# Kernel optimization log

Hardware: AMD Instinct MI355X
Metric: run time of the kernel (lower is better)

## Reference

```python
import jax, jax.numpy as jnp
import numpy as np

LEVEL_N = [81920, 20480, 5120, 1280, 320]  # faces at div..div-4 (div=6, 20*4^d)
K = 10  # SpherePHD conv kernel taps
W_SHAPES = [(64,3),(64,64),(128,64),(128,128),(256,128),(256,256),(256,256),(512,256),(512,512),(512,512),(512,512),(512,512),(512,512)]
BLOCKS = [[0,1],[2,3],[4,5,6],[7,8,9],[10,11,12]]  # conv indices per VGG block


def setup_inputs() -> dict:
    key = jax.random.key(0)
    ks = iter(jax.random.split(key, 64))
    d = {"x": jax.random.normal(next(ks), (2, 3, LEVEL_N[0]), jnp.float32)}
    for l, n in enumerate(LEVEL_N):
        d[f"conv_t{l}"] = jax.random.randint(next(ks), (n, K), 0, n, jnp.int32)
        d[f"adj_t{l}"] = jax.random.randint(next(ks), (n, 4), 0, n, jnp.int32)
        d[f"pool_t{l}"] = jax.random.randint(next(ks), (n // 4,), 0, n, jnp.int32)
    for i, (o, c) in enumerate(W_SHAPES):
        d[f"w{i}"] = jax.random.normal(next(ks), (o, c, K), jnp.float32) * (1.0 / np.sqrt(c * K))
        d[f"b{i}"] = jnp.zeros((o,), jnp.float32)
    return d


def phd_conv(x, w, b, table):
    # x: [B,C,N], table: [N,K] -> gather neighbors [B,C,N,K], weighted sum, ReLU
    g = x[:, :, table]
    y = jnp.einsum('bcnk,ock->bon', g, w) + b[None, :, None]
    return jax.nn.relu(y)


def phd_maxpool(x, adj, pool):
    # max over adjacent faces, then subsample to parent faces
    m = jnp.max(x[:, :, adj], axis=-1)  # [B,C,N]
    return m[:, :, pool]                # [B,C,N/4]


def reference(x, conv_t0, conv_t1, conv_t2, conv_t3, conv_t4,
              adj_t0, adj_t1, adj_t2, adj_t3, adj_t4,
              pool_t0, pool_t1, pool_t2, pool_t3, pool_t4,
              w0, w1, w2, w3, w4, w5, w6, w7, w8, w9, w10, w11, w12,
              b0, b1, b2, b3, b4, b5, b6, b7, b8, b9, b10, b11, b12):
    conv_ts = [conv_t0, conv_t1, conv_t2, conv_t3, conv_t4]
    adj_ts = [adj_t0, adj_t1, adj_t2, adj_t3, adj_t4]
    pool_ts = [pool_t0, pool_t1, pool_t2, pool_t3, pool_t4]
    ws = [w0, w1, w2, w3, w4, w5, w6, w7, w8, w9, w10, w11, w12]
    bs = [b0, b1, b2, b3, b4, b5, b6, b7, b8, b9, b10, b11, b12]
    h = x
    for lvl, idxs in enumerate(BLOCKS):
        for i in idxs:
            h = phd_conv(h, ws[i], bs[i], conv_ts[lvl])
        h = phd_maxpool(h, adj_ts[lvl], pool_ts[lvl])
    return h  # [2, 512, 80]
```

## Files before the change

kernel.cpp:

```cpp
#include <hip/hip_runtime.h>
#include <stdint.h>

typedef __bf16 bf16;
typedef bf16 bf16x8 __attribute__((ext_vector_type(8)));
typedef float f32x4 __attribute__((ext_vector_type(4)));
typedef unsigned short u16x8 __attribute__((ext_vector_type(8)));

__device__ __forceinline__ void gload_lds16(const bf16* g, bf16* l) {
    __builtin_amdgcn_global_load_lds(
        (const __attribute__((address_space(1))) void*)g,
        (__attribute__((address_space(3))) void*)l, 16, 0, 0);
}

template<int C>
__device__ __forceinline__ void cvt_pair(const float* __restrict__ src,
                                         bf16* __restrict__ dst,
                                         int tp, int base5)
{
    int ocp = tp - base5;
    int oc  = ocp * 2;
    int o   = oc / C;
    int c   = oc & (C - 1);
    const f32x4* s4 = (const f32x4*)(src + (size_t)oc * 10);
    float v[20];
#pragma unroll
    for (int j = 0; j < 5; j++) {
        f32x4 p = s4[j];
#pragma unroll
        for (int e = 0; e < 4; e++) v[4 * j + e] = p[e];
    }
    unsigned short* d = (unsigned short*)(dst + (size_t)base5 * 20
                                              + (size_t)o * 10 * C + c);
#pragma unroll
    for (int k = 0; k < 10; k++) {
        union { bf16 h; unsigned short u; } a, b;
        a.h = (bf16)v[k];
        b.h = (bf16)v[10 + k];
        uint32_t pk = (uint32_t)a.u | ((uint32_t)b.u << 16);
        *(uint32_t*)(d + (size_t)k * C) = pk;
    }
}

__global__ __launch_bounds__(256) void prep_w(
    const float* w1, const float* w2, const float* w3, const float* w4,
    const float* w5, const float* w6, const float* w7, const float* w8,
    const float* w9, const float* w10, const float* w11, const float* w12,
    bf16* __restrict__ dst)
{
    int t = blockIdx.x * 256 + threadIdx.x;
    if (t >= 817152) return;
    if      (t <   2048) cvt_pair< 64>(w1,  dst, t, 0);
    else if (t <   6144) cvt_pair< 64>(w2,  dst, t, 2048);
    else if (t <  14336) cvt_pair<128>(w3,  dst, t, 6144);
    else if (t <  30720) cvt_pair<128>(w4,  dst, t, 14336);
    else if (t <  63488) cvt_pair<256>(w5,  dst, t, 30720);
    else if (t <  96256) cvt_pair<256>(w6,  dst, t, 63488);
    else if (t < 161792) cvt_pair<256>(w7,  dst, t, 96256);
    else if (t < 292864) cvt_pair<512>(w8,  dst, t, 161792);
    else if (t < 423936) cvt_pair<512>(w9,  dst, t, 292864);
    else if (t < 555008) cvt_pair<512>(w10, dst, t, 423936);
    else if (t < 686080) cvt_pair<512>(w11, dst, t, 555008);
    else                 cvt_pair<512>(w12, dst, t, 686080);
}

__global__ __launch_bounds__(256) void conv0_kernel(
    const float* __restrict__ x, const float* __restrict__ w0,
    const float* __restrict__ b0, const int* __restrict__ table,
    bf16* __restrict__ out)
{
    const int N = 81920;
    __shared__ float wls[30][64];
    __shared__ float bls[64];
    int tid = threadIdx.x;
    for (int i = tid; i < 1920; i += 256) {
        int o = i / 30, ck = i - o * 30;
        wls[ck][o] = w0[i];
    }
    if (tid < 64) bls[tid] = b0[tid];
    __syncthreads();

    int p = blockIdx.x * 256 + tid;
    int b = p >= N;
    int n = p - b * N;
    int idx[10];
    const int* trow = table + n * 10;
#pragma unroll
    for (int k = 0; k < 10; k++) idx[k] = trow[k];
    float xv[30];
#pragma unroll
    for (int c = 0; c < 3; c++)
#pragma unroll
        for (int k = 0; k < 10; k++)
            xv[c * 10 + k] = x[(b * 3 + c) * N + idx[k]];

    float acc[64];
#pragma unroll
    for (int o = 0; o < 64; o++) acc[o] = bls[o];
    for (int ck = 0; ck < 30; ck++) {
        float xs = xv[ck];
        const f32x4* wrow = (const f32x4*)(&wls[ck][0]);
#pragma unroll
        for (int o4 = 0; o4 < 16; o4++) {
            f32x4 w4 = wrow[o4];
            acc[o4 * 4 + 0] += xs * w4[0];
            acc[o4 * 4 + 1] += xs * w4[1];
            acc[o4 * 4 + 2] += xs * w4[2];
            acc[o4 * 4 + 3] += xs * w4[3];
        }
    }
    bf16x8 ob[8];
#pragma unroll
    for (int i = 0; i < 8; i++)
#pragma unroll
        for (int e = 0; e < 8; e++)
            ob[i][e] = (bf16)fmaxf(acc[i * 8 + e], 0.0f);
    bf16x8* dst = (bf16x8*)(out + (size_t)p * 64);
#pragma unroll
    for (int i = 0; i < 8; i++) dst[i] = ob[i];
}

template<int C, int BP, int BO, int WO, int WP>
__global__ __launch_bounds__(256) void conv_p(
    const bf16* __restrict__ in, const bf16* __restrict__ w,
    const float* __restrict__ bias, const int* __restrict__ table,
    bf16* __restrict__ out, float* __restrict__ slab,
    int N, int O, int S, int PO)
{
    constexpr int CH = C / 64;
    constexpr int CHUNKS = CH * 10;
    constexpr int CK = C * 10;
    constexpr int TO = (BO / WO) / 16;
    constexpr int TP = (BP / WP) / 16;
    constexpr int XI = BP / 32;
    constexpr int WI = BO / 32;
    constexpr int LPS = XI + WI;
    static_assert(LPS == 8 || LPS == 6, "vmcnt literal");

    __shared__ bf16 Xs[3][BP][64];
    __shared__ bf16 Ws[3][BO][64];
    __shared__ int rowoff[BP][10];

    const int tid = threadIdx.x;
    const int lane = tid & 63;
    const int wid = tid >> 6;
    const int wo = wid & (WO - 1), wp = wid / WO;
    const int l16 = lane & 15, q = lane >> 4;

    const int p0 = blockIdx.x * BP;
    const int o0 = blockIdx.y * BO;
    const int z = blockIdx.z;

    for (int j = tid; j < BP * 10; j += 256) {
        int pp = j / 10, k = j - pp * 10;
        int p = p0 + pp;
        int b = p >= N;
        int n = p - b * N;
        rowoff[pp][k] = (b * N + table[n * 10 + k]) * C;
    }
    __syncthreads();

    int xsrow[XI], xgseg[XI];
#pragma unroll
    for (int t = 0; t < XI; t++) {
        int row = wid * (BP / 4) + t * 8 + (lane >> 3);
        xsrow[t] = row;
        xgseg[t] = (lane & 7) ^ (row & 7);
    }
    int wsrow[WI];
    const bf16* wbase[WI];
#pragma unroll
    for (int t = 0; t < WI; t++) {
        int row = wid * (BO / 4) + t * 8 + (lane >> 3);
        int gs = (lane & 7) ^ (row & 7);
        wsrow[t] = row;
        wbase[t] = w + (size_t)(o0 + row) * CK + gs * 8;
    }

    const int per = CHUNKS / S;
    const int c0chunk = z * per;

    auto stage = [&](int chunk, int b3) {
        int k = chunk / CH;
        int cofs = (chunk & (CH - 1)) * 64;
#pragma unroll
        for (int t = 0; t < XI; t++) {
            int ro = rowoff[xsrow[t]][k];
            gload_lds16(in + ro + cofs + xgseg[t] * 8,
                        &Xs[b3][wid * (BP / 4) + t * 8][0]);
        }
#pragma unroll
        for (int t = 0; t < WI; t++)
            gload_lds16(wbase[t] + chunk * 64,
                        &Ws[b3][wid * (BO / 4) + t * 8][0]);
    };

    f32x4 acc[TO][TP];
#pragma unroll
    for (int a = 0; a < TO; a++)
#pragma unroll
        for (int c = 0; c < TP; c++) acc[a][c] = (f32x4){0.f, 0.f, 0.f, 0.f};

    stage(c0chunk, 0);
    stage(c0chunk + 1, 1);

    const int obase = wo * (BO / WO);
    const int pbase = wp * (BP / WP);
    const int arow = obase + l16;
    const int brow = pbase + l16;
    const int sx = l16 & 7;

    int bi = 0, bs = 2;
    for (int i = 0; i < per; i++) {
        if constexpr (LPS == 8)
            asm volatile("s_waitcnt vmcnt(8)" ::: "memory");
        else
            asm volatile("s_waitcnt vmcnt(6)" ::: "memory");
        __builtin_amdgcn_s_barrier();
        const bf16* xb = &Xs[bi][0][0];
        const bf16* wb = &Ws[bi][0][0];
#pragma unroll
        for (int ks = 0; ks < 2; ks++) {
            int slot = ((ks * 4 + q) ^ sx) * 8;
            bf16x8 af[TO], bfr[TP];
#pragma unroll
            for (int to = 0; to < TO; to++)
                af[to] = *(const bf16x8*)(wb + (arow + to * 16) * 64 + slot);
#pragma unroll
            for (int tp = 0; tp < TP; tp++)
                bfr[tp] = *(const bf16x8*)(xb + (brow + tp * 16) * 64 + slot);
#pragma unroll
            for (int to = 0; to < TO; to++)
#pragma unroll
                for (int tp = 0; tp < TP; tp++)
                    acc[to][tp] = __builtin_amdgcn_mfma_f32_16x16x32_bf16(
                        af[to], bfr[tp], acc[to][tp], 0, 0, 0);
        }
        int nx = i + 2 < per ? i + 2 : per - 1;
        stage(c0chunk + nx, bs);
        bi = bi == 2 ? 0 : bi + 1;
        bs = bs == 2 ? 0 : bs + 1;
    }

    if (S == 1) {
#pragma unroll
        for (int to = 0; to < TO; ++to) {
            int ob = o0 + obase + to * 16 + q * 4;
            f32x4 bv = *(const f32x4*)(bias + ob);
#pragma unroll
            for (int tp = 0; tp < TP; ++tp) {
                int p = p0 + pbase + tp * 16 + l16;
                union { ushort4 u4; unsigned short s[4]; } pk;
#pragma unroll
                for (int r = 0; r < 4; r++) {
                    float v = fmaxf(acc[to][tp][r] + bv[r], 0.0f);
                    union { bf16 h; unsigned short u; } cc;
                    cc.h = (bf16)v;
                    pk.s[r] = cc.u;
                }
                *(ushort4*)(out + (size_t)p * O + ob) = pk.u4;
            }
        }
    } else {
        float* sb = slab + (size_t)z * PO;
#pragma unroll
        for (int to = 0; to < TO; ++to) {
            int ob = o0 + obase + to * 16 + q * 4;
#pragma unroll
            for (int tp = 0; tp < TP; ++tp) {
                int p = p0 + pbase + tp * 16 + l16;
                *(f32x4*)(sb + (size_t)p * O + ob) = acc[to][tp];
            }
        }
    }
}

__global__ __launch_bounds__(256) void epi_reduce(
    const float* __restrict__ slab, const float* __restrict__ bias,
    bf16* __restrict__ out, int PO, int Omask, int S)
{
    int t4 = (blockIdx.x * 256 + threadIdx.x) * 4;
    if (t4 >= PO) return;
    f32x4 s = *(const f32x4*)(slab + t4);
    for (int zz = 1; zz < S; zz++)
        s += *(const f32x4*)(slab + (size_t)zz * PO + t4);
    int o = t4 & Omask;
    f32x4 bv = *(const f32x4*)(bias + o);
    union { ushort4 u4; unsigned short e[4]; } pk;
#pragma unroll
    for (int r = 0; r < 4; r++) {
        float v = fmaxf(s[r] + bv[r], 0.0f);
        union { bf16 h; unsigned short u; } cc;
        cc.h = (bf16)v;
        pk.e[r] = cc.u;
    }
    *(ushort4*)((unsigned short*)out + t4) = pk.u4;
}

__global__ __launch_bounds__(256) void pool_kernel(
    const bf16* __restrict__ in, const int* __restrict__ adj,
    const int* __restrict__ pool, bf16* __restrict__ out,
    int N, int M, int c8shift)
{
    int t = blockIdx.x * 256 + threadIdx.x;
    int total = M << c8shift;
    if (t >= total) return;
    int cc = t & ((1 << c8shift) - 1);
    int j = t >> c8shift;
    int b = blockIdx.y;
    int C = 8 << c8shift;
    int s = pool[j];
    const int* a = adj + s * 4;
    const unsigned short* inu = (const unsigned short*)in;
    size_t base = (size_t)b * N * C + (size_t)cc * 8;
    u16x8 m = *(const u16x8*)(inu + base + (size_t)a[0] * C);
#pragma unroll
    for (int i = 1; i < 4; i++) {
        u16x8 v = *(const u16x8*)(inu + base + (size_t)a[i] * C);
#pragma unroll
        for (int e = 0; e < 8; e++) m[e] = v[e] > m[e] ? v[e] : m[e];
    }
    *(u16x8*)((unsigned short*)out + ((size_t)b * M + j) * C + (size_t)cc * 8) = m;
}

__global__ __launch_bounds__(256) void final_pool(
    const bf16* __restrict__ in, const int* __restrict__ adj,
    const int* __restrict__ pool, float* __restrict__ out)
{
    int t = blockIdx.x * 256 + threadIdx.x;
    if (t >= 81920) return;
    int j = t % 80;
    int rest = t / 80;
    int c = rest & 511;
    int b = rest >> 9;
    int s = pool[j];
    const int* a = adj + s * 4;
    float m = 0.0f;
#pragma unroll
    for (int i = 0; i < 4; i++) {
        float v = (float)in[((size_t)b * 320 + a[i]) * 512 + c];
        m = fmaxf(m, v);
    }
    out[t] = m;
}

extern "C" void kernel_launch(void* const* d_in, const int* in_sizes, int n_in,
                              void* d_out, int out_size, void* d_ws, size_t ws_size,
                              hipStream_t stream)
{
    const float* x = (const float*)d_in[0];
    const int* convT[5]; const int* adjT[5]; const int* poolT[5];
    for (int l = 0; l < 5; l++) {
        convT[l] = (const int*)d_in[1 + 3 * l];
        adjT[l]  = (const int*)d_in[2 + 3 * l];
        poolT[l] = (const int*)d_in[3 + 3 * l];
    }
    const float* W[13]; const float* Bs[13];
    for (int i = 0; i < 13; i++) {
        W[i]  = (const float*)d_in[16 + 2 * i];
        Bs[i] = (const float*)d_in[17 + 2 * i];
    }

    bf16* wbf   = (bf16*)d_ws;
    bf16* A     = (bf16*)((char*)d_ws + (40u << 20));
    bf16* Bb    = (bf16*)((char*)d_ws + (70u << 20));
    float* slabA = (float*)((char*)d_ws + (100u << 20));
    float* slabB = (float*)((char*)d_ws + (130u << 20));

    static const int woff[13] = {0, 0, 40960, 122880, 286720, 614400, 1269760,
                                 1925120, 3235840, 5857280, 8478720, 11100160, 13721600};

    prep_w<<<dim3(817152 / 256), dim3(256), 0, stream>>>(
        W[1], W[2], W[3], W[4], W[5], W[6], W[7], W[8], W[9], W[10], W[11], W[12], wbf);

    conv0_kernel<<<dim3(640), dim3(256), 0, stream>>>(x, W[0], Bs[0], convT[0], A);

    const int PO3 = 2560 * 512;
    const int PO4 = 640 * 512;

    conv_p<64, 128, 64, 1, 4><<<dim3(1280, 1, 1), dim3(256), 0, stream>>>(
        A, wbf + woff[1], Bs[1], convT[0], Bb, nullptr, 81920, 64, 1, 0);
    pool_kernel<<<dim3(640, 2), dim3(256), 0, stream>>>(Bb, adjT[0], poolT[0], A, 81920, 20480, 3);
    conv_p<64, 128, 128, 2, 2><<<dim3(320, 1, 1), dim3(256), 0, stream>>>(
        A, wbf + woff[2], Bs[2], convT[1], Bb, nullptr, 20480, 128, 1, 0);
    conv_p<128, 128, 128, 2, 2><<<dim3(320, 1, 1), dim3(256), 0, stream>>>(
        Bb, wbf + woff[3], Bs[3], convT[1], A, nullptr, 20480, 128, 1, 0);
    pool_kernel<<<dim3(320, 2), dim3(256), 0, stream>>>(A, adjT[1], poolT[1], Bb, 20480, 5120, 4);
    conv_p<128, 128, 128, 2, 2><<<dim3(80, 2, 1), dim3(256), 0, stream>>>(
        Bb, wbf + woff[4], Bs[4], convT[2], A, nullptr, 5120, 256, 1, 0);
    conv_p<256, 128, 128, 2, 2><<<dim3(80, 2, 1), dim3(256), 0, stream>>>(
        A, wbf + woff[5], Bs[5], convT[2], Bb, nullptr, 5120, 256, 1, 0);
    conv_p<256, 128, 128, 2, 2><<<dim3(80, 2, 1), dim3(256), 0, stream>>>(
        Bb, wbf + woff[6], Bs[6], convT[2], A, nullptr, 5120, 256, 1, 0);
    pool_kernel<<<dim3(160, 2), dim3(256), 0, stream>>>(A, adjT[2], poolT[2], Bb, 5120, 1280, 5);
    conv_p<256, 128, 128, 2, 2><<<dim3(20, 4, 2), dim3(256), 0, stream>>>(
        Bb, wbf + woff[7], Bs[7], convT[3], nullptr, slabA, 1280, 512, 2, PO3);
    epi_reduce<<<dim3(PO3 / 1024), dim3(256), 0, stream>>>(slabA, Bs[7], A, PO3, 511, 2);
    conv_p<512, 128, 128, 2, 2><<<dim3(20, 4, 2), dim3(256), 0, stream>>>(
        A, wbf + woff[8], Bs[8], convT[3], nullptr, slabB, 1280, 512, 2, PO3);
    epi_reduce<<<dim3(PO3 / 1024), dim3(256), 0, stream>>>(slabB, Bs[8], Bb, PO3, 511, 2);
    conv_p<512, 128, 128, 2, 2><<<dim3(20, 4, 2), dim3(256), 0, stream>>>(
        Bb, wbf + woff[9], Bs[9], convT[3], nullptr, slabA, 1280, 512, 2, PO3);
    epi_reduce<<<dim3(PO3 / 1024), dim3(256), 0, stream>>>(slabA, Bs[9], A, PO3, 511, 2);
    pool_kernel<<<dim3(80, 2), dim3(256), 0, stream>>>(A, adjT[3], poolT[3], Bb, 1280, 320, 6);
    conv_p<512, 128, 128, 2, 2><<<dim3(5, 4, 8), dim3(256), 0, stream>>>(
        Bb, wbf + woff[10], Bs[10], convT[4], nullptr, slabA, 320, 512, 8, PO4);
    epi_reduce<<<dim3(PO4 / 1024), dim3(256), 0, stream>>>(slabA, Bs[10], A, PO4, 511, 8);
    conv_p<512, 128, 128, 2, 2><<<dim3(5, 4, 8), dim3(256), 0, stream>>>(
        A, wbf + woff[11], Bs[11], convT[4], nullptr, slabB, 320, 512, 8, PO4);
    epi_reduce<<<dim3(PO4 / 1024), dim3(256), 0, stream>>>(slabB, Bs[11], Bb, PO4, 511, 8);
    conv_p<512, 128, 128, 2, 2><<<dim3(5, 4, 8), dim3(256), 0, stream>>>(
        Bb, wbf + woff[12], Bs[12], convT[4], nullptr, slabA, 320, 512, 8, PO4);
    epi_reduce<<<dim3(PO4 / 1024), dim3(256), 0, stream>>>(slabA, Bs[12], A, PO4, 511, 8);

    final_pool<<<dim3(320), dim3(256), 0, stream>>>(A, adjT[4], poolT[4], (float*)d_out);
}
```

Baseline: 623.9 us.

## Add register-direct conv kernel for level-0 layer and shrink conv_p tiles to 64x64

```diff
diff --git a/kernel.cpp b/kernel.cpp
--- a/kernel.cpp
+++ b/kernel.cpp
@@ -119,6 +119,100 @@
     for (int i = 0; i < 8; i++) dst[i] = ob[i];
 }
 
+struct Frags64 {
+    bf16x8 a[4][2];
+    bf16x8 b[2][2];
+};
+
+__global__ __launch_bounds__(256) void conv_reg64(
+    const bf16* __restrict__ in, const bf16* __restrict__ w,
+    const float* __restrict__ bias, const int* __restrict__ table,
+    bf16* __restrict__ out, int N)
+{
+    const int tid = threadIdx.x;
+    const int lane = tid & 63;
+    const int wid = tid >> 6;
+    const int l16 = lane & 15, q = lane >> 4;
+
+    const int p0 = blockIdx.x * 128 + wid * 32;
+
+    int nrow[2][10];
+#pragma unroll
+    for (int tp = 0; tp < 2; tp++) {
+        int p = p0 + tp * 16 + l16;
+        int b = p >= N;
+        int n = p - b * N;
+        const int* tr = table + n * 10;
+#pragma unroll
+        for (int k = 0; k < 10; k++)
+            nrow[tp][k] = (b * N + tr[k]) * 64;
+    }
+
+    const bf16* wbase[4];
+#pragma unroll
+    for (int to = 0; to < 4; to++)
+        wbase[to] = w + (to * 16 + l16) * 640 + q * 8;
+    const bf16* xq = in + q * 8;
+
+    f32x4 acc[4][2];
+#pragma unroll
+    for (int a = 0; a < 4; a++)
+#pragma unroll
+        for (int c = 0; c < 2; c++) acc[a][c] = (f32x4){0.f, 0.f, 0.f, 0.f};
+
+    auto loadF = [&](int k, Frags64& F) {
+#pragma unroll
+        for (int to = 0; to < 4; to++)
+#pragma unroll
+            for (int ks = 0; ks < 2; ks++)
+                F.a[to][ks] = *(const bf16x8*)(wbase[to] + k * 64 + ks * 32);
+#pragma unroll
+        for (int tp = 0; tp < 2; tp++)
+#pragma unroll
+            for (int ks = 0; ks < 2; ks++)
+                F.b[tp][ks] = *(const bf16x8*)(xq + nrow[tp][k] + ks * 32);
+    };
+    auto mm = [&](Frags64& F) {
+#pragma unroll
+        for (int ks = 0; ks < 2; ks++)
+#pragma unroll
+            for (int to = 0; to < 4; to++)
+#pragma unroll
+                for (int tp = 0; tp < 2; tp++)
+                    acc[to][tp] = __builtin_amdgcn_mfma_f32_16x16x32_bf16(
+                        F.a[to][ks], F.b[tp][ks], acc[to][tp], 0, 0, 0);
+    };
+
+    Frags64 F0, F1;
+    loadF(0, F0);
+#pragma unroll
+    for (int k = 0; k < 10; k += 2) {
+        loadF(k + 1, F1);
+        mm(F0);
+        if (k + 2 < 10) loadF(k + 2, F0);
+        mm(F1);
+    }
+
+#pragma unroll
+    for (int to = 0; to < 4; ++to) {
+        int ob = to * 16 + q * 4;
+        f32x4 bv = *(const f32x4*)(bias + ob);
+#pragma unroll
+        for (int tp = 0; tp < 2; ++tp) {
+            int p = p0 + tp * 16 + l16;
+            union { ushort4 u4; unsigned short s[4]; } pk;
+#pragma unroll
+            for (int r = 0; r < 4; r++) {
+                float v = fmaxf(acc[to][tp][r] + bv[r], 0.0f);
+                union { bf16 h; unsigned short u; } cc;
+                cc.h = (bf16)v;
+                pk.s[r] = cc.u;
+            }
+            *(ushort4*)(out + (size_t)p * 64 + ob) = pk.u4;
+        }
+    }
+}
+
 template<int C, int BP, int BO, int WO, int WP>
 __global__ __launch_bounds__(256) void conv_p(
     const bf16* __restrict__ in, const bf16* __restrict__ w,
@@ -134,7 +228,7 @@
     constexpr int XI = BP / 32;
     constexpr int WI = BO / 32;
     constexpr int LPS = XI + WI;
-    static_assert(LPS == 8 || LPS == 6, "vmcnt literal");
+    static_assert(LPS == 4, "vmcnt literal assumes 4 loads/stage");
 
     __shared__ bf16 Xs[3][BP][64];
     __shared__ bf16 Ws[3][BO][64];
@@ -166,13 +260,11 @@
         xsrow[t] = row;
         xgseg[t] = (lane & 7) ^ (row & 7);
     }
-    int wsrow[WI];
     const bf16* wbase[WI];
 #pragma unroll
     for (int t = 0; t < WI; t++) {
         int row = wid * (BO / 4) + t * 8 + (lane >> 3);
         int gs = (lane & 7) ^ (row & 7);
-        wsrow[t] = row;
         wbase[t] = w + (size_t)(o0 + row) * CK + gs * 8;
     }
 
@@ -211,10 +303,7 @@
 
     int bi = 0, bs = 2;
     for (int i = 0; i < per; i++) {
-        if constexpr (LPS == 8)
-            asm volatile("s_waitcnt vmcnt(8)" ::: "memory");
-        else
-            asm volatile("s_waitcnt vmcnt(6)" ::: "memory");
+        asm volatile("s_waitcnt vmcnt(4)" ::: "memory");
         __builtin_amdgcn_s_barrier();
         const bf16* xb = &Xs[bi][0][0];
         const bf16* wb = &Ws[bi][0][0];
@@ -377,38 +466,38 @@
     const int PO3 = 2560 * 512;
     const int PO4 = 640 * 512;
 
-    conv_p<64, 128, 64, 1, 4><<<dim3(1280, 1, 1), dim3(256), 0, stream>>>(
-        A, wbf + woff[1], Bs[1], convT[0], Bb, nullptr, 81920, 64, 1, 0);
+    conv_reg64<<<dim3(1280), dim3(256), 0, stream>>>(
+        A, wbf + woff[1], Bs[1], convT[0], Bb, 81920);
     pool_kernel<<<dim3(640, 2), dim3(256), 0, stream>>>(Bb, adjT[0], poolT[0], A, 81920, 20480, 3);
-    conv_p<64, 128, 128, 2, 2><<<dim3(320, 1, 1), dim3(256), 0, stream>>>(
+    conv_p<64, 64, 64, 2, 2><<<dim3(640, 2, 1), dim3(256), 0, stream>>>(
         A, wbf + woff[2], Bs[2], convT[1], Bb, nullptr, 20480, 128, 1, 0);
-    conv_p<128, 128, 128, 2, 2><<<dim3(320, 1, 1), dim3(256), 0, stream>>>(
+    conv_p<128, 64, 64, 2, 2><<<dim3(640, 2, 1), dim3(256), 0, stream>>>(
         Bb, wbf + woff[3], Bs[3], convT[1], A, nullptr, 20480, 128, 1, 0);
     pool_kernel<<<dim3(320, 2), dim3(256), 0, stream>>>(A, adjT[1], poolT[1], Bb, 20480, 5120, 4);
-    conv_p<128, 128, 128, 2, 2><<<dim3(80, 2, 1), dim3(256), 0, stream>>>(
+    conv_p<128, 64, 64, 2, 2><<<dim3(160, 4, 1), dim3(256), 0, stream>>>(
         Bb, wbf + woff[4], Bs[4], convT[2], A, nullptr, 5120, 256, 1, 0);
-    conv_p<256, 128, 128, 2, 2><<<dim3(80, 2, 1), dim3(256), 0, stream>>>(
+    conv_p<256, 64, 64, 2, 2><<<dim3(160, 4, 1), dim3(256), 0, stream>>>(
         A, wbf + woff[5], Bs[5], convT[2], Bb, nullptr, 5120, 256, 1, 0);
-    conv_p<256, 128, 128, 2, 2><<<dim3(80, 2, 1), dim3(256), 0, stream>>>(
+    conv_p<256, 64, 64, 2, 2><<<dim3(160, 4, 1), dim3(256), 0, stream>>>(
         Bb, wbf + woff[6], Bs[6], convT[2], A, nullptr, 5120, 256, 1, 0);
     pool_kernel<<<dim3(160, 2), dim3(256), 0, stream>>>(A, adjT[2], poolT[2], Bb, 5120, 1280, 5);
-    conv_p<256, 128, 128, 2, 2><<<dim3(20, 4, 2), dim3(256), 0, stream>>>(
+    conv_p<256, 64, 64, 2, 2><<<dim3(40, 8, 2), dim3(256), 0, stream>>>(
         Bb, wbf + woff[7], Bs[7], convT[3], nullptr, slabA, 1280, 512, 2, PO3);
     epi_reduce<<<dim3(PO3 / 1024), dim3(256), 0, stream>>>(slabA, Bs[7], A, PO3, 511, 2);
-    conv_p<512, 128, 128, 2, 2><<<dim3(20, 4, 2), dim3(256), 0, stream>>>(
+    conv_p<512, 64, 64, 2, 2><<<dim3(40, 8, 2), dim3(256), 0, stream>>>(
         A, wbf + woff[8], Bs[8], convT[3], nullptr, slabB, 1280, 512, 2, PO3);
     epi_reduce<<<dim3(PO3 / 1024), dim3(256), 0, stream>>>(slabB, Bs[8], Bb, PO3, 511, 2);
-    conv_p<512, 128, 128, 2, 2><<<dim3(20, 4, 2), dim3(256), 0, stream>>>(
+    conv_p<512, 64, 64, 2, 2><<<dim3(40, 8, 2), dim3(256), 0, stream>>>(
         Bb, wbf + woff[9], Bs[9], convT[3], nullptr, slabA, 1280, 512, 2, PO3);
     epi_reduce<<<dim3(PO3 / 1024), dim3(256), 0, stream>>>(slabA, Bs[9], A, PO3, 511, 2);
     pool_kernel<<<dim3(80, 2), dim3(256), 0, stream>>>(A, adjT[3], poolT[3], Bb, 1280, 320, 6);
-    conv_p<512, 128, 128, 2, 2><<<dim3(5, 4, 8), dim3(256), 0, stream>>>(
+    conv_p<512, 64, 64, 2, 2><<<dim3(10, 8, 8), dim3(256), 0, stream>>>(
         Bb, wbf + woff[10], Bs[10], convT[4], nullptr, slabA, 320, 512, 8, PO4);
     epi_reduce<<<dim3(PO4 / 1024), dim3(256), 0, stream>>>(slabA, Bs[10], A, PO4, 511, 8);
-    conv_p<512, 128, 128, 2, 2><<<dim3(5, 4, 8), dim3(256), 0, stream>>>(
+    conv_p<512, 64, 64, 2, 2><<<dim3(10, 8, 8), dim3(256), 0, stream>>>(
         A, wbf + woff[11], Bs[11], convT[4], nullptr, slabB, 320, 512, 8, PO4);
     epi_reduce<<<dim3(PO4 / 1024), dim3(256), 0, stream>>>(slabB, Bs[11], Bb, PO4, 511, 8);
-    conv_p<512, 128, 128, 2, 2><<<dim3(5, 4, 8), dim3(256), 0, stream>>>(
+    conv_p<512, 64, 64, 2, 2><<<dim3(10, 8, 8), dim3(256), 0, stream>>>(
         Bb, wbf + woff[12], Bs[12], convT[4], nullptr, slabA, 320, 512, 8, PO4);
     epi_reduce<<<dim3(PO4 / 1024), dim3(256), 0, stream>>>(slabA, Bs[12], A, PO4, 511, 8);
 
```

After: 559.4 us. -10.3%, faster.
